# Kernel tuning notes

Measured on AMD Instinct MI355X. Metric: run time of the kernel, lower is better.

The kernel has to match this reference:

```python
import jax, jax.numpy as jnp
import numpy as np
import math

B, L, DM = 2, 1024, 1024
DI = 2 * DM          # d_inner = expand * d_model
N = 16               # d_state
K = 4                # d_conv
R = math.ceil(DM / 16)  # dt_rank = 64


def setup_inputs() -> dict:
    key = jax.random.key(0)
    ks = jax.random.split(key, 10)
    s = 0.02
    x = jax.random.normal(ks[0], (B, L, DM), jnp.float32)
    W_in = jax.random.normal(ks[1], (DM, 2 * DI), jnp.float32) * s
    conv_w = jax.random.normal(ks[2], (DI, K), jnp.float32) * (1.0 / math.sqrt(K))
    conv_b = jnp.zeros((DI,), jnp.float32)
    W_x = jax.random.normal(ks[3], (DI, R + 2 * N), jnp.float32) * s
    dt_std = R ** (-0.5)
    W_dt = jax.random.uniform(ks[4], (R, DI), jnp.float32, -dt_std, dt_std)
    # dt bias init so softplus(bias) in [dt_min, dt_max]
    u = jax.random.uniform(ks[5], (DI,), jnp.float32)
    dt = jnp.exp(u * (math.log(0.1) - math.log(0.001)) + math.log(0.001))
    dt = jnp.clip(dt, 0.0001, None)
    b_dt = dt + jnp.log(-jnp.expm1(-dt))
    A_log = jnp.log(jnp.broadcast_to(jnp.arange(1, N + 1, dtype=jnp.float32), (DI, N)))
    D_param = jnp.ones((DI,), jnp.float32)
    W_out = jax.random.normal(ks[6], (DI, DM), jnp.float32) * s
    return {"x": x, "W_in": W_in, "conv_w": conv_w, "conv_b": conv_b,
            "W_x": W_x, "W_dt": W_dt, "b_dt": b_dt, "A_log": A_log,
            "D_param": D_param, "W_out": W_out}


def reference(x, W_in, conv_w, conv_b, W_x, W_dt, b_dt, A_log, D_param, W_out):
    b, l, _ = x.shape
    k = conv_w.shape[1]
    n = A_log.shape[1]
    r = W_dt.shape[0]

    xz = x @ W_in                                  # (b,l,2*DI)
    xs, z = jnp.split(xz, 2, axis=-1)              # each (b,l,DI)

    # causal depthwise conv1d (padding = k-1 on the left, truncated to l)
    xp = jnp.pad(xs, ((0, 0), (k - 1, 0), (0, 0)))
    x_conv = conv_b + sum(conv_w[:, j] * xp[:, j:j + l, :] for j in range(k))
    x_conv = jax.nn.silu(x_conv)

    A = -jnp.exp(A_log)                            # (DI,n)
    x_dbl = x_conv @ W_x                           # (b,l,r+2n)
    dt_low, Bm, Cm = jnp.split(x_dbl, [r, r + n], axis=-1)
    dt = jax.nn.softplus(dt_low @ W_dt + b_dt)     # (b,l,DI)

    def step(h, inp):
        dt_t, B_t, C_t, u_t = inp                  # (b,DI),(b,n),(b,n),(b,DI)
        A_bar = jnp.exp(dt_t[:, :, None] * A)      # (b,DI,n)
        h = A_bar * h + (dt_t[:, :, None] * B_t[:, None, :]) * u_t[:, :, None]
        y = jnp.einsum('bdn,bn->bd', h, C_t)
        return h, y

    T = lambda a: jnp.swapaxes(a, 0, 1)            # (b,l,...) -> (l,b,...)
    h0 = jnp.zeros((b, dt.shape[-1], n), x.dtype)
    h_final, ys = jax.lax.scan(step, h0, (T(dt), T(Bm), T(Cm), T(x_conv)))
    y = T(ys) + D_param * x_conv                   # (b,l,DI)

    y = y * jax.nn.silu(z)
    out = y @ W_out                                # (b,l,DM)
    conv_cache = jnp.swapaxes(xs[:, -k:, :], 1, 2) # (b,DI,k)
    return out, h_final, conv_cache
```

## Files before the change

kernel.cpp:

```cpp
#include <hip/hip_runtime.h>
#include <hip/hip_bf16.h>

#define MROWS 2048
#define DMOD 1024
#define DINNER 2048
#define NSTATE 16
#define KCONV 4
#define RRANK 64
#define NX 96
#define NXP 128

#define CCH 64
#define TCH 16

typedef __attribute__((ext_vector_type(8))) short bf16x8;
typedef __attribute__((ext_vector_type(4))) float f32x4;

__device__ inline short f2bf(float f) {
    return (short)__builtin_bit_cast(unsigned short, __float2bfloat16(f));
}

__global__ __launch_bounds__(256) void cast_bf16_kernel(const float* __restrict__ in,
                                                        short* __restrict__ out, int n4) {
    int i = blockIdx.x * 256 + threadIdx.x;
    if (i < n4) {
        float4 v = ((const float4*)in)[i];
        short4 o;
        o.x = f2bf(v.x); o.y = f2bf(v.y); o.z = f2bf(v.z); o.w = f2bf(v.w);
        ((short4*)out)[i] = o;
    }
}

__global__ void transpose_cast_kernel(const float* __restrict__ W, short* __restrict__ WT,
                                      int Kdim, int Ndim, int NdimP) {
    __shared__ float tile[32][33];
    int n0 = blockIdx.x * 32, k0 = blockIdx.y * 32;
    int x = threadIdx.x;
    for (int y = threadIdx.y; y < 32; y += 8) {
        int kk = k0 + y, nn = n0 + x;
        tile[y][x] = (nn < Ndim) ? W[(size_t)kk * Ndim + nn] : 0.f;
    }
    __syncthreads();
    for (int y = threadIdx.y; y < 32; y += 8) {
        int nn = n0 + y, kk = k0 + x;
        if (nn < NdimP) WT[(size_t)nn * Kdim + kk] = f2bf(tile[x][y]);
    }
}

__global__ __launch_bounds__(256) void gemm_bf16_v2(const short* __restrict__ A,
                                                    const short* __restrict__ BT,
                                                    float* __restrict__ C,
                                                    int M, int Kdim, int Nstore, int Kper) {
    __shared__ __align__(16) short As[128][40];
    __shared__ __align__(16) short Bs[64][40];
    int tid = threadIdx.x;
    int m0 = blockIdx.y * 128, n0 = blockIdx.x * 64;
    int kbase = blockIdx.z * Kper;
    int wave = tid >> 6, lane = tid & 63;
    int wr = wave >> 1, wc = wave & 1;
    int lrow = lane & 15, quad = lane >> 4;

    int arow = tid >> 1, acol = (tid & 1) * 16;
    int brow = tid >> 2, bcol = (tid & 3) * 8;

    const uint4* gA = (const uint4*)(A + (size_t)(m0 + arow) * Kdim + kbase + acol);
    const uint4* gB = (const uint4*)(BT + (size_t)(n0 + brow) * Kdim + kbase + bcol);

    f32x4 acc[4][2] = {};

    for (int k0 = 0; k0 < Kper; k0 += 32) {
        uint4 a0 = gA[0], a1 = gA[1];
        uint4 b0 = gB[0];
        gA += 4; gB += 4;
        *(uint4*)&As[arow][acol]     = a0;
        *(uint4*)&As[arow][acol + 8] = a1;
        *(uint4*)&Bs[brow][bcol]     = b0;
        __syncthreads();

        bf16x8 af[4], bf2[2];
#pragma unroll
        for (int i = 0; i < 4; i++)
            af[i] = *(const bf16x8*)&As[wr * 64 + i * 16 + lrow][quad * 8];
#pragma unroll
        for (int j = 0; j < 2; j++)
            bf2[j] = *(const bf16x8*)&Bs[wc * 32 + j * 16 + lrow][quad * 8];
#pragma unroll
        for (int i = 0; i < 4; i++)
#pragma unroll
            for (int j = 0; j < 2; j++)
                acc[i][j] = __builtin_amdgcn_mfma_f32_16x16x32_bf16(af[i], bf2[j], acc[i][j], 0, 0, 0);
        __syncthreads();
    }

    float* Cz = C + (size_t)blockIdx.z * M * Nstore;
#pragma unroll
    for (int i = 0; i < 4; i++) {
#pragma unroll
        for (int j = 0; j < 2; j++) {
            int col = n0 + wc * 32 + j * 16 + lrow;
            if (col < Nstore) {
                int rbase = m0 + wr * 64 + i * 16 + quad * 4;
#pragma unroll
                for (int r = 0; r < 4; r++)
                    Cz[(size_t)(rbase + r) * Nstore + col] = acc[i][j][r];
            }
        }
    }
}

__global__ __launch_bounds__(256) void reduce2_kernel(const float* __restrict__ p,
                                                      float* __restrict__ out, int n4) {
    int i = blockIdx.x * 256 + threadIdx.x;
    if (i < n4) {
        float4 a = ((const float4*)p)[i];
        float4 b = ((const float4*)p)[i + n4];
        float4 o;
        o.x = a.x + b.x; o.y = a.y + b.y; o.z = a.z + b.z; o.w = a.w + b.w;
        ((float4*)out)[i] = o;
    }
}

__global__ __launch_bounds__(256) void reduce8_kernel(const float* __restrict__ p,
                                                      float* __restrict__ xdbl) {
    int i = blockIdx.x * 256 + threadIdx.x;
    int c = i & 127;
    int m = i >> 7;
    if (c < NX) {
        float s = 0.f;
#pragma unroll
        for (int kz = 0; kz < 8; kz++)
            s += p[(size_t)kz * MROWS * NXP + i];
        xdbl[(size_t)m * NX + c] = s;
    }
}

__global__ __launch_bounds__(256) void conv_silu_kernel(const float* __restrict__ xz,
                                                        const float* __restrict__ conv_w,
                                                        const float* __restrict__ conv_b,
                                                        float* __restrict__ xconv,
                                                        short* __restrict__ xconv_bf) {
    int idx = blockIdx.x * 256 + threadIdx.x;
    int d = idx & (DINNER - 1);
    int m = idx >> 11;
    int t = m & 1023, b = m >> 10;
    float4 w = *(const float4*)&conv_w[d * 4];
    float acc = conv_b[d];
    int base = b << 10;
#pragma unroll
    for (int j = 0; j < 4; j++) {
        int tt = t - 3 + j;
        if (tt >= 0) {
            float wj = (j == 0) ? w.x : (j == 1) ? w.y : (j == 2) ? w.z : w.w;
            acc += wj * xz[((size_t)(base + tt) << 12) + d];
        }
    }
    float s = acc / (1.f + __expf(-acc));
    xconv[idx] = s;
    xconv_bf[idx] = f2bf(s);
}

__global__ __launch_bounds__(256) void conv_cache_kernel(const float* __restrict__ xz,
                                                         float* __restrict__ out) {
    int i = blockIdx.x * 256 + threadIdx.x;
    if (i >= 2 * DINNER * KCONV) return;
    int j = i & 3;
    int d = (i >> 2) & (DINNER - 1);
    int b = i >> 13;
    out[i] = xz[((size_t)(b * 1024 + 1020 + j) << 12) + d];
}

__global__ __launch_bounds__(256) void dt_kernel(const float* __restrict__ xdbl,
                                                 const float* __restrict__ Wdt,
                                                 const float* __restrict__ bdt,
                                                 float* __restrict__ dt) {
    __shared__ float dl[16][64];
    int tid = threadIdx.x;
    int m0 = blockIdx.y * 16;
    int d = blockIdx.x * 256 + tid;
    {
        int r = tid >> 4;
        int k = (tid & 15) * 4;
        float4 v = *(const float4*)&xdbl[(size_t)(m0 + r) * NX + k];
        *(float4*)&dl[r][k] = v;
    }
    __syncthreads();
    float acc[16] = {};
    for (int k = 0; k < 64; k++) {
        float w = Wdt[(size_t)k * DINNER + d];
#pragma unroll
        for (int m = 0; m < 16; m++) acc[m] += dl[m][k] * w;
    }
    float bias = bdt[d];
#pragma unroll
    for (int m = 0; m < 16; m++) {
        float v = acc[m] + bias;
        float sp = (v > 20.f) ? v : log1pf(__expf(v));
        dt[(size_t)(m0 + m) * DINNER + d] = sp;
    }
}

__global__ __launch_bounds__(256) void scan_phase1_kernel(const float* __restrict__ dt,
                                                          const float* __restrict__ xconv,
                                                          const float* __restrict__ xdbl,
                                                          const float* __restrict__ A_log,
                                                          float* __restrict__ Pbuf,
                                                          float* __restrict__ hpart) {
    int i = blockIdx.x * 256 + threadIdx.x;
    int ch = i & 4095;
    int chunk = i >> 12;
    int d = ch & (DINNER - 1);
    int b = ch >> 11;
    float a[16];
#pragma unroll
    for (int q = 0; q < 4; q++) {
        float4 v = *(const float4*)&A_log[d * 16 + q * 4];
        a[q*4+0] = -__expf(v.x); a[q*4+1] = -__expf(v.y);
        a[q*4+2] = -__expf(v.z); a[q*4+3] = -__expf(v.w);
    }
    float h[16] = {};
    float sdt = 0.f;
    size_t rowbase = ((size_t)b << 10) + chunk * TCH;
#pragma unroll 4
    for (int t = 0; t < TCH; t++) {
        size_t row = rowbase + t;
        float dtv = dt[(row << 11) + d];
        float u   = xconv[(row << 11) + d];
        float du = dtv * u;
        float Bv[16];
#pragma unroll
        for (int q = 0; q < 4; q++)
            *(float4*)&Bv[q*4] = *(const float4*)&xdbl[row * NX + RRANK + q * 4];
        sdt += dtv;
#pragma unroll
        for (int n = 0; n < 16; n++) {
            float ab = __expf(dtv * a[n]);
            h[n] = ab * h[n] + du * Bv[n];
        }
    }
    float P[16];
#pragma unroll
    for (int n = 0; n < 16; n++) P[n] = __expf(sdt * a[n]);
    size_t o = (size_t)i * 16;
#pragma unroll
    for (int q = 0; q < 4; q++) {
        *(float4*)&hpart[o + q*4] = *(float4*)&h[q*4];
        *(float4*)&Pbuf[o + q*4]  = *(float4*)&P[q*4];
    }
}

__global__ __launch_bounds__(256) void scan_combine_kernel(float* __restrict__ Pbuf,
                                                           const float* __restrict__ hpart,
                                                           float* __restrict__ hfin) {
    int i = blockIdx.x * 256 + threadIdx.x;
    float carry = 0.f;
#pragma unroll 8
    for (int c = 0; c < CCH; c++) {
        size_t idx = ((size_t)c << 16) + i;
        float P  = Pbuf[idx];
        float hp = hpart[idx];
        Pbuf[idx] = carry;
        carry = P * carry + hp;
    }
    hfin[i] = carry;
}

__global__ __launch_bounds__(256) void scan_phase3_kernel(const float* __restrict__ dt,
                                                          const float* __restrict__ xconv,
                                                          const float* __restrict__ xdbl,
                                                          const float* __restrict__ xz,
                                                          const float* __restrict__ A_log,
                                                          const float* __restrict__ Dp,
                                                          const float* __restrict__ hin,
                                                          short* __restrict__ ygate) {
    int i = blockIdx.x * 256 + threadIdx.x;
    int ch = i & 4095;
    int chunk = i >> 12;
    int d = ch & (DINNER - 1);
    int b = ch >> 11;
    float a[16];
#pragma unroll
    for (int q = 0; q < 4; q++) {
        float4 v = *(const float4*)&A_log[d * 16 + q * 4];
        a[q*4+0] = -__expf(v.x); a[q*4+1] = -__expf(v.y);
        a[q*4+2] = -__expf(v.z); a[q*4+3] = -__expf(v.w);
    }
    float h[16];
#pragma unroll
    for (int q = 0; q < 4; q++)
        *(float4*)&h[q*4] = *(const float4*)&hin[(size_t)i * 16 + q * 4];
    float Dv = Dp[d];
    size_t rowbase = ((size_t)b << 10) + chunk * TCH;
#pragma unroll 4
    for (int t = 0; t < TCH; t++) {
        size_t row = rowbase + t;
        float dtv = dt[(row << 11) + d];
        float u   = xconv[(row << 11) + d];
        float zv  = xz[(row << 12) + DINNER + d];
        float du = dtv * u;
        float Bv[16], Cv[16];
#pragma unroll
        for (int q = 0; q < 4; q++) {
            *(float4*)&Bv[q*4] = *(const float4*)&xdbl[row * NX + RRANK + q * 4];
            *(float4*)&Cv[q*4] = *(const float4*)&xdbl[row * NX + RRANK + NSTATE + q * 4];
        }
        float y = 0.f;
#pragma unroll
        for (int n = 0; n < 16; n++) {
            float ab = __expf(dtv * a[n]);
            h[n] = ab * h[n] + du * Bv[n];
            y += h[n] * Cv[n];
        }
        float sg = zv / (1.f + __expf(-zv));
        ygate[(row << 11) + d] = f2bf((y + Dv * u) * sg);
    }
}

extern "C" void kernel_launch(void* const* d_in, const int* in_sizes, int n_in,
                              void* d_out, int out_size, void* d_ws, size_t ws_size,
                              hipStream_t stream) {
    const float* x      = (const float*)d_in[0];
    const float* W_in   = (const float*)d_in[1];
    const float* conv_w = (const float*)d_in[2];
    const float* conv_b = (const float*)d_in[3];
    const float* W_x    = (const float*)d_in[4];
    const float* W_dt   = (const float*)d_in[5];
    const float* b_dt   = (const float*)d_in[6];
    const float* A_log  = (const float*)d_in[7];
    const float* D_par  = (const float*)d_in[8];
    const float* W_out  = (const float*)d_in[9];

    float* out = (float*)d_out;
    float* hfin = out + 2 * 1024 * 1024;
    float* ccache = hfin + 2 * DINNER * NSTATE;

    char* ws = (char*)d_ws;
    float* xz       = (float*)ws;                 ws += (size_t)MROWS * 4096 * 4;
    float* xconv    = (float*)ws;                 ws += (size_t)MROWS * DINNER * 4;
    float* dtbuf    = (float*)ws;                 ws += (size_t)MROWS * DINNER * 4;
    float* xdbl     = (float*)ws;                 ws += (size_t)MROWS * NX * 4;
    short* xconv_bf = (short*)ws;                 ws += (size_t)MROWS * DINNER * 2;
    short* ygate    = (short*)ws;                 ws += (size_t)MROWS * DINNER * 2;
    short* x_bf     = (short*)ws;                 ws += (size_t)MROWS * DMOD * 2;
    short* WinT     = (short*)ws;                 ws += (size_t)4096 * DMOD * 2;
    short* WxT      = (short*)ws;                 ws += (size_t)NXP * DINNER * 2;
    short* WoutT    = (short*)ws;                 ws += (size_t)DMOD * DINNER * 2;
    float* Pbuf     = (float*)ws;                 ws += (size_t)CCH * 4096 * 16 * 4;
    float* hpart    = (float*)ws;                 ws += (size_t)CCH * 4096 * 16 * 4;

    float* Cp2 = (float*)WinT;
    float* Cp3 = (float*)xz;
    float* hinb = Pbuf;

    cast_bf16_kernel<<<(MROWS * DMOD / 4 + 255) / 256, 256, 0, stream>>>(x, x_bf, MROWS * DMOD / 4);
    transpose_cast_kernel<<<dim3(4096 / 32, DMOD / 32), dim3(32, 8), 0, stream>>>(W_in, WinT, DMOD, 4096, 4096);
    transpose_cast_kernel<<<dim3(NXP / 32, DINNER / 32), dim3(32, 8), 0, stream>>>(W_x, WxT, DINNER, NX, NXP);
    transpose_cast_kernel<<<dim3(DMOD / 32, DINNER / 32), dim3(32, 8), 0, stream>>>(W_out, WoutT, DINNER, DMOD, DMOD);

    gemm_bf16_v2<<<dim3(4096 / 64, MROWS / 128, 1), 256, 0, stream>>>(x_bf, WinT, xz, MROWS, DMOD, 4096, DMOD);

    conv_silu_kernel<<<MROWS * DINNER / 256, 256, 0, stream>>>(xz, conv_w, conv_b, xconv, xconv_bf);
    conv_cache_kernel<<<(2 * DINNER * KCONV + 255) / 256, 256, 0, stream>>>(xz, ccache);

    gemm_bf16_v2<<<dim3(NXP / 64, MROWS / 128, 8), 256, 0, stream>>>(xconv_bf, WxT, Cp2, MROWS, DINNER, NXP, DINNER / 8);
    reduce8_kernel<<<MROWS * NXP / 256, 256, 0, stream>>>(Cp2, xdbl);

    dt_kernel<<<dim3(DINNER / 256, MROWS / 16), 256, 0, stream>>>(xdbl, W_dt, b_dt, dtbuf);

    scan_phase1_kernel<<<CCH * 4096 / 256, 256, 0, stream>>>(dtbuf, xconv, xdbl, A_log, Pbuf, hpart);
    scan_combine_kernel<<<4096 * 16 / 256, 256, 0, stream>>>(Pbuf, hpart, hfin);
    scan_phase3_kernel<<<CCH * 4096 / 256, 256, 0, stream>>>(dtbuf, xconv, xdbl, xz, A_log, D_par, hinb, ygate);

    gemm_bf16_v2<<<dim3(DMOD / 64, MROWS / 128, 2), 256, 0, stream>>>(ygate, WoutT, Cp3, MROWS, DINNER, DMOD, DINNER / 2);
    reduce2_kernel<<<(MROWS * DMOD / 4 + 255) / 256, 256, 0, stream>>>(Cp3, out, MROWS * DMOD / 4);
}
```

Baseline: 292.3 us.

## Use 128x128 GEMM tiles with direct global-to-LDS loads and rebalance split-K

Replaces the GEMM with a 128x128 tile kernel that loads A and B straight into LDS through global_load_lds, removing the register staging step. Each wave now computes 4x4 MFMA tiles, which raises reuse of the data it loads. Split-K grows to 16 for the x_proj GEMM and to 4 for the out_proj GEMM, with matching reduce kernels, and conv_cache is folded into the conv_silu kernel. In exchange it drops the LDS row padding, which risks bank conflicts, and it adds a separate workspace buffer for the larger partial sums.

```diff
diff --git a/kernel.cpp b/kernel.cpp
--- a/kernel.cpp
+++ b/kernel.cpp
@@ -20,6 +20,12 @@
     return (short)__builtin_bit_cast(unsigned short, __float2bfloat16(f));
 }
 
+__device__ __forceinline__ void gll16(const void* gp, void* lp) {
+    __builtin_amdgcn_global_load_lds(
+        (const __attribute__((address_space(1))) void*)gp,
+        (__attribute__((address_space(3))) void*)lp, 16, 0, 0);
+}
+
 __global__ __launch_bounds__(256) void cast_bf16_kernel(const float* __restrict__ in,
                                                         short* __restrict__ out, int n4) {
     int i = blockIdx.x * 256 + threadIdx.x;
@@ -47,48 +53,47 @@
     }
 }
 
-__global__ __launch_bounds__(256) void gemm_bf16_v2(const short* __restrict__ A,
-                                                    const short* __restrict__ BT,
-                                                    float* __restrict__ C,
-                                                    int M, int Kdim, int Nstore, int Kper) {
-    __shared__ __align__(16) short As[128][40];
-    __shared__ __align__(16) short Bs[64][40];
+__global__ __launch_bounds__(256) void gemm_m97(const short* __restrict__ A,
+                                                const short* __restrict__ BT,
+                                                float* __restrict__ C,
+                                                int M, int Kdim, int Nstore, int Kper) {
+    __shared__ __align__(16) short As[128][32];
+    __shared__ __align__(16) short Bs[128][32];
     int tid = threadIdx.x;
-    int m0 = blockIdx.y * 128, n0 = blockIdx.x * 64;
+    int m0 = blockIdx.y * 128, n0 = blockIdx.x * 128;
     int kbase = blockIdx.z * Kper;
     int wave = tid >> 6, lane = tid & 63;
     int wr = wave >> 1, wc = wave & 1;
     int lrow = lane & 15, quad = lane >> 4;
 
-    int arow = tid >> 1, acol = (tid & 1) * 16;
-    int brow = tid >> 2, bcol = (tid & 3) * 8;
-
-    const uint4* gA = (const uint4*)(A + (size_t)(m0 + arow) * Kdim + kbase + acol);
-    const uint4* gB = (const uint4*)(BT + (size_t)(n0 + brow) * Kdim + kbase + bcol);
-
-    f32x4 acc[4][2] = {};
+    int srow = wave * 16 + (lane >> 2);
+    int scol = (lane & 3) * 8;
+    const short* gA = A + (size_t)(m0 + srow) * Kdim + kbase + scol;
+    const short* gB = BT + (size_t)(n0 + srow) * Kdim + kbase + scol;
+
+    f32x4 acc[4][4] = {};
 
     for (int k0 = 0; k0 < Kper; k0 += 32) {
-        uint4 a0 = gA[0], a1 = gA[1];
-        uint4 b0 = gB[0];
-        gA += 4; gB += 4;
-        *(uint4*)&As[arow][acol]     = a0;
-        *(uint4*)&As[arow][acol + 8] = a1;
-        *(uint4*)&Bs[brow][bcol]     = b0;
+#pragma unroll
+        for (int c = 0; c < 2; c++) {
+            gll16(gA + (size_t)c * 64 * Kdim, &As[(c * 4 + wave) * 16][0]);
+            gll16(gB + (size_t)c * 64 * Kdim, &Bs[(c * 4 + wave) * 16][0]);
+        }
+        gA += 32; gB += 32;
         __syncthreads();
 
-        bf16x8 af[4], bf2[2];
+        bf16x8 af[4], bf4[4];
 #pragma unroll
         for (int i = 0; i < 4; i++)
             af[i] = *(const bf16x8*)&As[wr * 64 + i * 16 + lrow][quad * 8];
 #pragma unroll
-        for (int j = 0; j < 2; j++)
-            bf2[j] = *(const bf16x8*)&Bs[wc * 32 + j * 16 + lrow][quad * 8];
+        for (int j = 0; j < 4; j++)
+            bf4[j] = *(const bf16x8*)&Bs[wc * 64 + j * 16 + lrow][quad * 8];
 #pragma unroll
         for (int i = 0; i < 4; i++)
 #pragma unroll
-            for (int j = 0; j < 2; j++)
-                acc[i][j] = __builtin_amdgcn_mfma_f32_16x16x32_bf16(af[i], bf2[j], acc[i][j], 0, 0, 0);
+            for (int j = 0; j < 4; j++)
+                acc[i][j] = __builtin_amdgcn_mfma_f32_16x16x32_bf16(af[i], bf4[j], acc[i][j], 0, 0, 0);
         __syncthreads();
     }
 
@@ -96,8 +101,8 @@
 #pragma unroll
     for (int i = 0; i < 4; i++) {
 #pragma unroll
-        for (int j = 0; j < 2; j++) {
-            int col = n0 + wc * 32 + j * 16 + lrow;
+        for (int j = 0; j < 4; j++) {
+            int col = n0 + wc * 64 + j * 16 + lrow;
             if (col < Nstore) {
                 int rbase = m0 + wr * 64 + i * 16 + quad * 4;
 #pragma unroll
@@ -108,27 +113,29 @@
     }
 }
 
-__global__ __launch_bounds__(256) void reduce2_kernel(const float* __restrict__ p,
+__global__ __launch_bounds__(256) void reduce4_kernel(const float* __restrict__ p,
                                                       float* __restrict__ out, int n4) {
     int i = blockIdx.x * 256 + threadIdx.x;
     if (i < n4) {
-        float4 a = ((const float4*)p)[i];
-        float4 b = ((const float4*)p)[i + n4];
-        float4 o;
-        o.x = a.x + b.x; o.y = a.y + b.y; o.z = a.z + b.z; o.w = a.w + b.w;
+        float4 o = ((const float4*)p)[i];
+#pragma unroll
+        for (int z = 1; z < 4; z++) {
+            float4 a = ((const float4*)p)[i + (size_t)z * n4];
+            o.x += a.x; o.y += a.y; o.z += a.z; o.w += a.w;
+        }
         ((float4*)out)[i] = o;
     }
 }
 
-__global__ __launch_bounds__(256) void reduce8_kernel(const float* __restrict__ p,
-                                                      float* __restrict__ xdbl) {
+__global__ __launch_bounds__(256) void reduce16_kernel(const float* __restrict__ p,
+                                                       float* __restrict__ xdbl) {
     int i = blockIdx.x * 256 + threadIdx.x;
     int c = i & 127;
     int m = i >> 7;
     if (c < NX) {
         float s = 0.f;
 #pragma unroll
-        for (int kz = 0; kz < 8; kz++)
+        for (int kz = 0; kz < 16; kz++)
             s += p[(size_t)kz * MROWS * NXP + i];
         xdbl[(size_t)m * NX + c] = s;
     }
@@ -138,7 +145,8 @@
                                                         const float* __restrict__ conv_w,
                                                         const float* __restrict__ conv_b,
                                                         float* __restrict__ xconv,
-                                                        short* __restrict__ xconv_bf) {
+                                                        short* __restrict__ xconv_bf,
+                                                        float* __restrict__ ccache) {
     int idx = blockIdx.x * 256 + threadIdx.x;
     int d = idx & (DINNER - 1);
     int m = idx >> 11;
@@ -157,16 +165,12 @@
     float s = acc / (1.f + __expf(-acc));
     xconv[idx] = s;
     xconv_bf[idx] = f2bf(s);
-}
-
-__global__ __launch_bounds__(256) void conv_cache_kernel(const float* __restrict__ xz,
-                                                         float* __restrict__ out) {
-    int i = blockIdx.x * 256 + threadIdx.x;
-    if (i >= 2 * DINNER * KCONV) return;
-    int j = i & 3;
-    int d = (i >> 2) & (DINNER - 1);
-    int b = i >> 13;
-    out[i] = xz[((size_t)(b * 1024 + 1020 + j) << 12) + d];
+    if (idx < 2 * DINNER * KCONV) {
+        int j = idx & 3;
+        int dd = (idx >> 2) & (DINNER - 1);
+        int bb = idx >> 13;
+        ccache[idx] = xz[((size_t)(bb * 1024 + 1020 + j) << 12) + dd];
+    }
 }
 
 __global__ __launch_bounds__(256) void dt_kernel(const float* __restrict__ xdbl,
@@ -346,8 +350,8 @@
     short* WoutT    = (short*)ws;                 ws += (size_t)DMOD * DINNER * 2;
     float* Pbuf     = (float*)ws;                 ws += (size_t)CCH * 4096 * 16 * 4;
     float* hpart    = (float*)ws;                 ws += (size_t)CCH * 4096 * 16 * 4;
-
-    float* Cp2 = (float*)WinT;
+    float* Cp2      = (float*)ws;                 ws += (size_t)16 * MROWS * NXP * 4;
+
     float* Cp3 = (float*)xz;
     float* hinb = Pbuf;
 
@@ -356,13 +360,12 @@
     transpose_cast_kernel<<<dim3(NXP / 32, DINNER / 32), dim3(32, 8), 0, stream>>>(W_x, WxT, DINNER, NX, NXP);
     transpose_cast_kernel<<<dim3(DMOD / 32, DINNER / 32), dim3(32, 8), 0, stream>>>(W_out, WoutT, DINNER, DMOD, DMOD);
 
-    gemm_bf16_v2<<<dim3(4096 / 64, MROWS / 128, 1), 256, 0, stream>>>(x_bf, WinT, xz, MROWS, DMOD, 4096, DMOD);
-
-    conv_silu_kernel<<<MROWS * DINNER / 256, 256, 0, stream>>>(xz, conv_w, conv_b, xconv, xconv_bf);
-    conv_cache_kernel<<<(2 * DINNER * KCONV + 255) / 256, 256, 0, stream>>>(xz, ccache);
-
-    gemm_bf16_v2<<<dim3(NXP / 64, MROWS / 128, 8), 256, 0, stream>>>(xconv_bf, WxT, Cp2, MROWS, DINNER, NXP, DINNER / 8);
-    reduce8_kernel<<<MROWS * NXP / 256, 256, 0, stream>>>(Cp2, xdbl);
+    gemm_m97<<<dim3(4096 / 128, MROWS / 128, 1), 256, 0, stream>>>(x_bf, WinT, xz, MROWS, DMOD, 4096, DMOD);
+
+    conv_silu_kernel<<<MROWS * DINNER / 256, 256, 0, stream>>>(xz, conv_w, conv_b, xconv, xconv_bf, ccache);
+
+    gemm_m97<<<dim3(1, MROWS / 128, 16), 256, 0, stream>>>(xconv_bf, WxT, Cp2, MROWS, DINNER, NXP, DINNER / 16);
+    reduce16_kernel<<<MROWS * NXP / 256, 256, 0, stream>>>(Cp2, xdbl);
 
     dt_kernel<<<dim3(DINNER / 256, MROWS / 16), 256, 0, stream>>>(xdbl, W_dt, b_dt, dtbuf);
 
@@ -370,6 +373,6 @@
     scan_combine_kernel<<<4096 * 16 / 256, 256, 0, stream>>>(Pbuf, hpart, hfin);
     scan_phase3_kernel<<<CCH * 4096 / 256, 256, 0, stream>>>(dtbuf, xconv, xdbl, xz, A_log, D_par, hinb, ygate);
 
-    gemm_bf16_v2<<<dim3(DMOD / 64, MROWS / 128, 2), 256, 0, stream>>>(ygate, WoutT, Cp3, MROWS, DINNER, DMOD, DINNER / 2);
-    reduce2_kernel<<<(MROWS * DMOD / 4 + 255) / 256, 256, 0, stream>>>(Cp3, out, MROWS * DMOD / 4);
-}
+    gemm_m97<<<dim3(DMOD / 128, MROWS / 128, 4), 256, 0, stream>>>(ygate, WoutT, Cp3, MROWS, DINNER, DMOD, DINNER / 4);
+    reduce4_kernel<<<(MROWS * DMOD / 4 + 255) / 256, 256, 0, stream>>>(Cp3, out, MROWS * DMOD / 4);
+}
```

After: 283.5 us. 1.03x faster.
